# Performance work log

Measured on AMD Instinct MI355X. Metric: run time of the kernel, lower is better.

## Reference

```python
import jax, jax.numpy as jnp
import numpy as np

B, T, D = 4096, 256, 64          # batch, steps, state_dim
LD, CD = 4, 8                    # latent_dim, categorical_dim
H = 32                           # mlp_hidden
FEAT = D + LD * CD               # fc1 input dim


def setup_inputs() -> dict:
    key = jax.random.key(0)
    ks = jax.random.split(key, 8)
    states = jax.random.normal(ks[0], (B, T, D), dtype=jnp.float32)
    # pre-sampled Gumbel(0,1) noise, as used inside F.gumbel_softmax
    u = jax.random.uniform(ks[1], (B, T, LD, CD), jnp.float32, 1e-6, 1.0 - 1e-6)
    gumbel = -jnp.log(-jnp.log(u))
    tau = jnp.float32(1.0)
    def lin(k, fan_in, fan_out):
        bound = 1.0 / np.sqrt(fan_in)
        kw, kb = jax.random.split(k)
        W = jax.random.uniform(kw, (fan_in, fan_out), jnp.float32, -bound, bound)
        b = jax.random.uniform(kb, (fan_out,), jnp.float32, -bound, bound)
        return W, b
    W1, b1 = lin(ks[2], FEAT, H)
    W2, b2 = lin(ks[3], H, H)
    W3, b3 = lin(ks[4], H, LD * CD)
    return {"states": states, "gumbel": gumbel, "tau": tau,
            "W1": W1, "b1": b1, "W2": W2, "b2": b2, "W3": W3, "b3": b3}


def reference(states, gumbel, tau, W1, b1, W2, b2, W3, b3):
    Bs, T, _ = states.shape
    ld, cd = gumbel.shape[2], gumbel.shape[3]
    # init_states: eye(cd)[0] tiled latent_dim times -> [B, ld*cd]
    c0 = jnp.tile(jax.nn.one_hot(0, cd, dtype=states.dtype), (Bs, ld))
    xs = (jnp.swapaxes(states, 0, 1), jnp.swapaxes(gumbel, 0, 1))  # [T,B,...]

    def step(c, x):
        s, g = x                                   # s:[B,D], g:[B,ld,cd]
        z = jnp.concatenate([s, c], axis=-1)       # [B, FEAT]
        h1 = jax.nn.relu(z @ W1 + b1)
        h2 = jax.nn.relu(h1 @ W2 + b2)
        q = (h2 @ W3 + b3).reshape(Bs, ld, cd)
        y_soft = jax.nn.softmax((q + g) / tau, axis=-1)
        # hard=True (eval mode) straight-through one-hot
        y_hard = jax.nn.one_hot(jnp.argmax(y_soft, axis=-1), cd, dtype=y_soft.dtype)
        y = y_hard + y_soft - jax.lax.stop_gradient(y_soft)
        c_new = y.reshape(Bs, ld * cd)
        return c_new, c_new

    _, out = jax.lax.scan(step, c0, xs)            # [T, B, ld*cd]
    return jnp.swapaxes(out, 0, 1)                 # [B, T, ld*cd]
```

## Files before the change

### kernel.cpp

```cpp
#include <hip/hip_runtime.h>

#define NB   4096
#define NT   256
#define ND   64

template <int CTRL>
__device__ __forceinline__ float dppf(float x) {
  return __int_as_float(__builtin_amdgcn_update_dpp(
      0, __float_as_int(x), CTRL, 0xF, 0xF, true));
}
__device__ __forceinline__ float bperm(int addr, float x) {
  return __int_as_float(__builtin_amdgcn_ds_bpermute(addr, __float_as_int(x)));
}
__device__ __forceinline__ float max8(float x) {
  float t = fmaxf(x, dppf<0xB1>(x));
  t = fmaxf(t, dppf<0x4E>(t));
  t = fmaxf(t, dppf<0x141>(t));
  return t;
}

__device__ __forceinline__ float mac16(float v, const float w[16], float init) {
  float a0 = fmaf(v, w[0], init);
  float a1 = dppf<0x121>(v) * w[1];
  a0 = fmaf(dppf<0x122>(v), w[2], a0);
  a1 = fmaf(dppf<0x123>(v), w[3], a1);
  a0 = fmaf(dppf<0x124>(v), w[4], a0);
  a1 = fmaf(dppf<0x125>(v), w[5], a1);
  a0 = fmaf(dppf<0x126>(v), w[6], a0);
  a1 = fmaf(dppf<0x127>(v), w[7], a1);
  a0 = fmaf(dppf<0x128>(v), w[8], a0);
  a1 = fmaf(dppf<0x129>(v), w[9], a1);
  a0 = fmaf(dppf<0x12A>(v), w[10], a0);
  a1 = fmaf(dppf<0x12B>(v), w[11], a1);
  a0 = fmaf(dppf<0x12C>(v), w[12], a0);
  a1 = fmaf(dppf<0x12D>(v), w[13], a1);
  a0 = fmaf(dppf<0x12E>(v), w[14], a0);
  a1 = fmaf(dppf<0x12F>(v), w[15], a1);
  return a0 + a1;
}

__global__ __launch_bounds__(256)
void h1pre_kernel(const float* __restrict__ S,
                  const float* __restrict__ W1,
                  const float* __restrict__ b1,
                  float* __restrict__ out) {
  const size_t row = (size_t)blockIdx.x * 256 + threadIdx.x;
  const float4* srow = (const float4*)(S + row * ND);

  float acc[32];
#pragma unroll
  for (int j = 0; j < 32; ++j) acc[j] = b1[j];

#pragma unroll 1
  for (int kc = 0; kc < 4; ++kc) {
    float4 x[4];
#pragma unroll
    for (int i = 0; i < 4; ++i) x[i] = srow[kc * 4 + i];
#pragma unroll
    for (int i = 0; i < 4; ++i) {
      const float xv[4] = {x[i].x, x[i].y, x[i].z, x[i].w};
#pragma unroll
      for (int kk = 0; kk < 4; ++kk) {
        const int k = kc * 16 + i * 4 + kk;
#pragma unroll
        for (int j = 0; j < 32; ++j)
          acc[j] = fmaf(xv[kk], W1[k * 32 + j], acc[j]);
      }
    }
  }

  float4* orow = (float4*)(out + row * 32);
#pragma unroll
  for (int q = 0; q < 8; ++q)
    orow[q] = make_float4(acc[4*q], acc[4*q+1], acc[4*q+2], acc[4*q+3]);
}

__global__ __launch_bounds__(256, 4)
void rec_kernel(const float* __restrict__ G,
                const float* __restrict__ W1,
                const float* __restrict__ W2,
                const float* __restrict__ b2,
                const float* __restrict__ W3,
                const float* __restrict__ b3,
                float* __restrict__ out) {
  const int tid  = threadIdx.x;
  const int wave = tid >> 6;
  const int lane = tid & 63;
  const int s    = lane & 15;
  const int g    = lane >> 4;
  const int jh   = g & 1;
  const int kh   = g >> 1;
  const int j    = s + 16 * jh;
  const int b    = blockIdx.x * 4 + wave;
  const bool lo  = (lane < 32);

  float w1[16], w2[16], w3[16];
#pragma unroll
  for (int r = 0; r < 16; ++r) {
    const int k = ((s - r) & 15) + 16 * kh;
    w1[r] = W1[(64 + k) * 32 + j];
    w2[r] = W2[k * 32 + j];
    w3[r] = W3[k * 32 + j];
  }
  const float bias2 = lo ? b2[j] : 0.f;
  const float bias3 = lo ? b3[j] : 0.f;

  const int a_x32 = (lane ^ 32) << 2;
  const int a_rd  = (s + 16 * kh) << 2;

  float v = (s % 8 == 0) ? 1.f : 0.f;

  const size_t base = ((size_t)b * NT) * 32 + (lane & 31);
  float hA = out[base], hB = out[base + 32];
  float gA = G[base],   gB = G[base + 32];

  const int sh = lane & 56;
  const int my = lane & 7;

#pragma unroll 1
  for (int t = 0; t < NT; ++t) {
    const int tp = (t + 2 < NT) ? t + 2 : NT - 1;
    const float hC = out[base + (size_t)tp * 32];
    const float gC = G[base + (size_t)tp * 32];

    const float p1 = mac16(v, w1, lo ? hA : 0.f);
    float q = p1 + bperm(a_x32, p1);
    v = bperm(a_rd, fmaxf(q, 0.f));

    const float p2 = mac16(v, w2, bias2);
    q = p2 + bperm(a_x32, p2);
    v = bperm(a_rd, fmaxf(q, 0.f));

    const float p3 = mac16(v, w3, lo ? (bias3 + gA) : 0.f);
    q = p3 + bperm(a_x32, p3);

    const float m = max8(q);
    const unsigned long long bl = __ballot(q == m);
    const unsigned gr = (unsigned)(bl >> sh) & 255u;
    const float y = ((__ffs(gr) - 1) == my) ? 1.f : 0.f;

    if (lo) out[base + (size_t)t * 32] = y;

    v = bperm(a_rd, y);

    hA = hB; hB = hC; gA = gB; gB = gC;
  }
}

extern "C" void kernel_launch(void* const* d_in, const int* in_sizes, int n_in,
                              void* d_out, int out_size, void* d_ws, size_t ws_size,
                              hipStream_t stream) {
  const float* S  = (const float*)d_in[0];
  const float* G  = (const float*)d_in[1];
  const float* W1 = (const float*)d_in[3];
  const float* b1 = (const float*)d_in[4];
  const float* W2 = (const float*)d_in[5];
  const float* b2 = (const float*)d_in[6];
  const float* W3 = (const float*)d_in[7];
  const float* b3 = (const float*)d_in[8];
  float* out = (float*)d_out;

  hipLaunchKernelGGL(h1pre_kernel, dim3((NB * NT) / 256), dim3(256), 0, stream,
                     S, W1, b1, out);
  hipLaunchKernelGGL(rec_kernel, dim3(NB / 4), dim3(256), 0, stream,
                     G, W1, W2, b2, W3, b3, out);
}
```

Baseline: 756.1 us.

## Replace ds_bpermute reductions with permlane16/32 swaps via remapped lane roles

Swaps the roles of the k-half and j-half lane groups so the partial-sum reduction becomes a cross-16-lane swap and the broadcast of the activation vector becomes a cross-32-lane swap with masking. This lets the recurrence use the permlane16_swap/permlane32_swap builtins, falling back to ds_swizzle or ds_bpermute, in place of LDS-routed bpermute ops on the serial critical path of every time step. The point is to cut per-step cross-lane communication latency. The cost is a more intricate lane mapping, where correctness depends on the keep and init_row masking.

```diff
diff --git a/kernel.cpp b/kernel.cpp
--- a/kernel.cpp
+++ b/kernel.cpp
@@ -9,9 +9,28 @@
   return __int_as_float(__builtin_amdgcn_update_dpp(
       0, __float_as_int(x), CTRL, 0xF, 0xF, true));
 }
-__device__ __forceinline__ float bperm(int addr, float x) {
-  return __int_as_float(__builtin_amdgcn_ds_bpermute(addr, __float_as_int(x)));
+
+__device__ __forceinline__ float sum_xor16(float x) {
+#if __has_builtin(__builtin_amdgcn_permlane16_swap)
+  auto r = __builtin_amdgcn_permlane16_swap(__float_as_int(x), __float_as_int(x),
+                                            false, false);
+  return __int_as_float((int)r[0]) + __int_as_float((int)r[1]);
+#else
+  return x + __int_as_float(__builtin_amdgcn_ds_swizzle(__float_as_int(x), 0x401F));
+#endif
 }
+
+__device__ __forceinline__ float sum_xor32(float x, int lane) {
+#if __has_builtin(__builtin_amdgcn_permlane32_swap)
+  auto r = __builtin_amdgcn_permlane32_swap(__float_as_int(x), __float_as_int(x),
+                                            false, false);
+  return __int_as_float((int)r[0]) + __int_as_float((int)r[1]);
+#else
+  return x + __int_as_float(
+      __builtin_amdgcn_ds_bpermute((lane ^ 32) << 2, __float_as_int(x)));
+#endif
+}
+
 __device__ __forceinline__ float max8(float x) {
   float t = fmaxf(x, dppf<0xB1>(x));
   t = fmaxf(t, dppf<0x4E>(t));
@@ -88,11 +107,12 @@
   const int lane = tid & 63;
   const int s    = lane & 15;
   const int g    = lane >> 4;
-  const int jh   = g & 1;
-  const int kh   = g >> 1;
+  const int kh   = g & 1;
+  const int jh   = g >> 1;
   const int j    = s + 16 * jh;
   const int b    = blockIdx.x * 4 + wave;
-  const bool lo  = (lane < 32);
+  const bool init_row = (kh == 0);
+  const bool keep     = (g == 0) | (g == 3);
 
   float w1[16], w2[16], w3[16];
 #pragma unroll
@@ -102,15 +122,12 @@
     w2[r] = W2[k * 32 + j];
     w3[r] = W3[k * 32 + j];
   }
-  const float bias2 = lo ? b2[j] : 0.f;
-  const float bias3 = lo ? b3[j] : 0.f;
-
-  const int a_x32 = (lane ^ 32) << 2;
-  const int a_rd  = (s + 16 * kh) << 2;
+  const float bias2 = init_row ? b2[j] : 0.f;
+  const float bias3 = init_row ? b3[j] : 0.f;
 
   float v = (s % 8 == 0) ? 1.f : 0.f;
 
-  const size_t base = ((size_t)b * NT) * 32 + (lane & 31);
+  const size_t base = ((size_t)b * NT) * 32 + j;
   float hA = out[base], hB = out[base + 32];
   float gA = G[base],   gB = G[base + 32];
 
@@ -123,25 +140,25 @@
     const float hC = out[base + (size_t)tp * 32];
     const float gC = G[base + (size_t)tp * 32];
 
-    const float p1 = mac16(v, w1, lo ? hA : 0.f);
-    float q = p1 + bperm(a_x32, p1);
-    v = bperm(a_rd, fmaxf(q, 0.f));
+    float p = mac16(v, w1, init_row ? hA : 0.f);
+    float q = sum_xor16(p);
+    v = sum_xor32(keep ? fmaxf(q, 0.f) : 0.f, lane);
 
-    const float p2 = mac16(v, w2, bias2);
-    q = p2 + bperm(a_x32, p2);
-    v = bperm(a_rd, fmaxf(q, 0.f));
+    p = mac16(v, w2, bias2);
+    q = sum_xor16(p);
+    v = sum_xor32(keep ? fmaxf(q, 0.f) : 0.f, lane);
 
-    const float p3 = mac16(v, w3, lo ? (bias3 + gA) : 0.f);
-    q = p3 + bperm(a_x32, p3);
+    p = mac16(v, w3, init_row ? (bias3 + gA) : 0.f);
+    q = sum_xor16(p);
 
     const float m = max8(q);
     const unsigned long long bl = __ballot(q == m);
     const unsigned gr = (unsigned)(bl >> sh) & 255u;
     const float y = ((__ffs(gr) - 1) == my) ? 1.f : 0.f;
 
-    if (lo) out[base + (size_t)t * 32] = y;
+    if (init_row) out[base + (size_t)t * 32] = y;
 
-    v = bperm(a_rd, y);
+    v = sum_xor32(keep ? y : 0.f, lane);
 
     hA = hB; hB = hC; gA = gB; gB = gC;
   }
```

Result: no change. 765.4 us (+1.2%).

## Pack two batch rows per wave, replacing bpermute reductions with swizzle exchange

Applied to the files above, without the earlier changes.

Each wave now processes two batch elements, one per 32-lane half, instead of one element spread across four 16-lane groups. Each lane owns one output neuron and computes its full 32-wide dot product from its own 16 activations plus the other 16-lane group's activations, fetched with a single ds_swizzle. This removes the two ds_bpermute round trips (partial-sum combine and redistribution) per layer and halves the grid. In exchange each lane holds twice as many weight registers, and the occupancy hint drops to 2 blocks per CU.

```diff
diff --git a/kernel.cpp b/kernel.cpp
--- a/kernel.cpp
+++ b/kernel.cpp
@@ -9,9 +9,11 @@
   return __int_as_float(__builtin_amdgcn_update_dpp(
       0, __float_as_int(x), CTRL, 0xF, 0xF, true));
 }
-__device__ __forceinline__ float bperm(int addr, float x) {
-  return __int_as_float(__builtin_amdgcn_ds_bpermute(addr, __float_as_int(x)));
+
+__device__ __forceinline__ float xchg16(float v) {
+  return __int_as_float(__builtin_amdgcn_ds_swizzle(__float_as_int(v), 0x401F));
 }
+
 __device__ __forceinline__ float max8(float x) {
   float t = fmaxf(x, dppf<0xB1>(x));
   t = fmaxf(t, dppf<0x4E>(t));
@@ -19,24 +21,42 @@
   return t;
 }
 
-__device__ __forceinline__ float mac16(float v, const float w[16], float init) {
-  float a0 = fmaf(v, w[0], init);
-  float a1 = dppf<0x121>(v) * w[1];
-  a0 = fmaf(dppf<0x122>(v), w[2], a0);
-  a1 = fmaf(dppf<0x123>(v), w[3], a1);
-  a0 = fmaf(dppf<0x124>(v), w[4], a0);
-  a1 = fmaf(dppf<0x125>(v), w[5], a1);
-  a0 = fmaf(dppf<0x126>(v), w[6], a0);
-  a1 = fmaf(dppf<0x127>(v), w[7], a1);
-  a0 = fmaf(dppf<0x128>(v), w[8], a0);
-  a1 = fmaf(dppf<0x129>(v), w[9], a1);
-  a0 = fmaf(dppf<0x12A>(v), w[10], a0);
-  a1 = fmaf(dppf<0x12B>(v), w[11], a1);
-  a0 = fmaf(dppf<0x12C>(v), w[12], a0);
-  a1 = fmaf(dppf<0x12D>(v), w[13], a1);
-  a0 = fmaf(dppf<0x12E>(v), w[14], a0);
-  a1 = fmaf(dppf<0x12F>(v), w[15], a1);
-  return a0 + a1;
+__device__ __forceinline__ float mac32(float v, float vB,
+                                       const float wo[16], const float wx[16],
+                                       float init) {
+  float c0 = fmaf(v, wo[0], init);
+  float c1 = dppf<0x121>(v) * wo[1];
+  float d0 = vB * wx[0];
+  float d1 = dppf<0x121>(vB) * wx[1];
+  c0 = fmaf(dppf<0x122>(v),  wo[2],  c0);
+  c1 = fmaf(dppf<0x123>(v),  wo[3],  c1);
+  d0 = fmaf(dppf<0x122>(vB), wx[2],  d0);
+  d1 = fmaf(dppf<0x123>(vB), wx[3],  d1);
+  c0 = fmaf(dppf<0x124>(v),  wo[4],  c0);
+  c1 = fmaf(dppf<0x125>(v),  wo[5],  c1);
+  d0 = fmaf(dppf<0x124>(vB), wx[4],  d0);
+  d1 = fmaf(dppf<0x125>(vB), wx[5],  d1);
+  c0 = fmaf(dppf<0x126>(v),  wo[6],  c0);
+  c1 = fmaf(dppf<0x127>(v),  wo[7],  c1);
+  d0 = fmaf(dppf<0x126>(vB), wx[6],  d0);
+  d1 = fmaf(dppf<0x127>(vB), wx[7],  d1);
+  c0 = fmaf(dppf<0x128>(v),  wo[8],  c0);
+  c1 = fmaf(dppf<0x129>(v),  wo[9],  c1);
+  d0 = fmaf(dppf<0x128>(vB), wx[8],  d0);
+  d1 = fmaf(dppf<0x129>(vB), wx[9],  d1);
+  c0 = fmaf(dppf<0x12A>(v),  wo[10], c0);
+  c1 = fmaf(dppf<0x12B>(v),  wo[11], c1);
+  d0 = fmaf(dppf<0x12A>(vB), wx[10], d0);
+  d1 = fmaf(dppf<0x12B>(vB), wx[11], d1);
+  c0 = fmaf(dppf<0x12C>(v),  wo[12], c0);
+  c1 = fmaf(dppf<0x12D>(v),  wo[13], c1);
+  d0 = fmaf(dppf<0x12C>(vB), wx[12], d0);
+  d1 = fmaf(dppf<0x12D>(vB), wx[13], d1);
+  c0 = fmaf(dppf<0x12E>(v),  wo[14], c0);
+  c1 = fmaf(dppf<0x12F>(v),  wo[15], c1);
+  d0 = fmaf(dppf<0x12E>(vB), wx[14], d0);
+  d1 = fmaf(dppf<0x12F>(vB), wx[15], d1);
+  return (c0 + c1) + (d0 + d1);
 }
 
 __global__ __launch_bounds__(256)
@@ -75,7 +95,7 @@
     orow[q] = make_float4(acc[4*q], acc[4*q+1], acc[4*q+2], acc[4*q+3]);
 }
 
-__global__ __launch_bounds__(256, 4)
+__global__ __launch_bounds__(256, 2)
 void rec_kernel(const float* __restrict__ G,
                 const float* __restrict__ W1,
                 const float* __restrict__ W2,
@@ -86,31 +106,30 @@
   const int tid  = threadIdx.x;
   const int wave = tid >> 6;
   const int lane = tid & 63;
+  const int half = lane >> 5;
+  const int l    = lane & 31;
   const int s    = lane & 15;
-  const int g    = lane >> 4;
-  const int jh   = g & 1;
-  const int kh   = g >> 1;
-  const int j    = s + 16 * jh;
-  const int b    = blockIdx.x * 4 + wave;
-  const bool lo  = (lane < 32);
+  const int rw   = (lane >> 4) & 1;
+  const int b    = (blockIdx.x * 4 + wave) * 2 + half;
 
-  float w1[16], w2[16], w3[16];
+  float w1o[16], w1x[16], w2o[16], w2x[16], w3o[16], w3x[16];
 #pragma unroll
   for (int r = 0; r < 16; ++r) {
-    const int k = ((s - r) & 15) + 16 * kh;
-    w1[r] = W1[(64 + k) * 32 + j];
-    w2[r] = W2[k * 32 + j];
-    w3[r] = W3[k * 32 + j];
+    const int kO = ((s - r) & 15) + 16 * rw;
+    const int kX = ((s - r) & 15) + 16 * (1 - rw);
+    w1o[r] = W1[(64 + kO) * 32 + l];
+    w1x[r] = W1[(64 + kX) * 32 + l];
+    w2o[r] = W2[kO * 32 + l];
+    w2x[r] = W2[kX * 32 + l];
+    w3o[r] = W3[kO * 32 + l];
+    w3x[r] = W3[kX * 32 + l];
   }
-  const float bias2 = lo ? b2[j] : 0.f;
-  const float bias3 = lo ? b3[j] : 0.f;
+  const float b2l = b2[l];
+  const float b3l = b3[l];
 
-  const int a_x32 = (lane ^ 32) << 2;
-  const int a_rd  = (s + 16 * kh) << 2;
+  float v = ((l & 7) == 0) ? 1.f : 0.f;
 
-  float v = (s % 8 == 0) ? 1.f : 0.f;
-
-  const size_t base = ((size_t)b * NT) * 32 + (lane & 31);
+  const size_t base = ((size_t)b * NT) * 32 + l;
   float hA = out[base], hB = out[base + 32];
   float gA = G[base],   gB = G[base + 32];
 
@@ -123,25 +142,24 @@
     const float hC = out[base + (size_t)tp * 32];
     const float gC = G[base + (size_t)tp * 32];
 
-    const float p1 = mac16(v, w1, lo ? hA : 0.f);
-    float q = p1 + bperm(a_x32, p1);
-    v = bperm(a_rd, fmaxf(q, 0.f));
+    float vB = xchg16(v);
+    float p  = mac32(v, vB, w1o, w1x, hA);
+    v  = fmaxf(p, 0.f);
 
-    const float p2 = mac16(v, w2, bias2);
-    q = p2 + bperm(a_x32, p2);
-    v = bperm(a_rd, fmaxf(q, 0.f));
+    vB = xchg16(v);
+    p  = mac32(v, vB, w2o, w2x, b2l);
+    v  = fmaxf(p, 0.f);
 
-    const float p3 = mac16(v, w3, lo ? (bias3 + gA) : 0.f);
-    q = p3 + bperm(a_x32, p3);
+    vB = xchg16(v);
+    const float q = mac32(v, vB, w3o, w3x, b3l + gA);
 
     const float m = max8(q);
     const unsigned long long bl = __ballot(q == m);
     const unsigned gr = (unsigned)(bl >> sh) & 255u;
     const float y = ((__ffs(gr) - 1) == my) ? 1.f : 0.f;
 
-    if (lo) out[base + (size_t)t * 32] = y;
-
-    v = bperm(a_rd, y);
+    out[base + (size_t)t * 32] = y;
+    v = y;
 
     hA = hB; hB = hC; gA = gB; gB = gC;
   }
@@ -162,6 +180,6 @@
 
   hipLaunchKernelGGL(h1pre_kernel, dim3((NB * NT) / 256), dim3(256), 0, stream,
                      S, W1, b1, out);
-  hipLaunchKernelGGL(rec_kernel, dim3(NB / 4), dim3(256), 0, stream,
+  hipLaunchKernelGGL(rec_kernel, dim3(NB / 8), dim3(256), 0, stream,
                      G, W1, W2, b2, W3, b3, out);
 }
```

Result: faster. 737.4 us (-2.5%).
